# Performance work log

Measured on AMD Instinct MI355X. Metric: run time of the kernel, lower is better.

Reference implementation:

```python
import jax, jax.numpy as jnp
import numpy as np


def setup_inputs() -> dict:
    key = jax.random.key(0)
    k1, k2, k3 = jax.random.split(key, 3)
    N, F, C, E = 100000, 256, 64, 3200000
    x = jax.random.normal(k1, (N, F), dtype=jnp.float32)
    edge_index = jax.random.randint(k2, (2, E), 0, N, dtype=jnp.int64)
    W = jax.random.normal(k3, (F, C), dtype=jnp.float32) * (1.0 / np.sqrt(F))
    b = jnp.zeros((C,), dtype=jnp.float32)
    return {"x": x, "edge_index": edge_index, "W": W, "b": b}


def reference(x, edge_index, W, b):
    N = x.shape[0]
    # Linear transform first (GCNConv: x @ W)
    xw = x @ W  # [N, C]
    # gcn_norm: add self-loops with weight 1
    loops = jnp.arange(N, dtype=edge_index.dtype)
    src = jnp.concatenate([edge_index[0], loops])
    dst = jnp.concatenate([edge_index[1], loops])
    ones = jnp.ones(src.shape[0], dtype=xw.dtype)
    deg = jax.ops.segment_sum(ones, dst, num_segments=N)  # in-degree incl. self-loop
    deg_inv_sqrt = jnp.where(deg > 0, jax.lax.rsqrt(deg), 0.0)
    norm = deg_inv_sqrt[src] * deg_inv_sqrt[dst]  # [E+N]
    # Message: norm * x_j, then MEAN aggregation over destinations (aggr='mean')
    msg = xw[src] * norm[:, None]  # [E+N, C]
    agg = jax.ops.segment_sum(msg, dst, num_segments=N)  # [N, C]
    cnt = jnp.maximum(deg, 1.0)  # number of incoming messages per node
    out = agg / cnt[:, None] + b
    return jax.nn.log_softmax(out, axis=1)
```

## Files before the change

### kernel.cpp

```cpp
#include <hip/hip_runtime.h>


#define C_DIM 64
#define F_DIM 256
#define TILE 128
#define BIN_PT 16
#define BIN_TILE_E 4096
#define SORT_CAP 6144

#if __has_builtin(__builtin_amdgcn_cvt_pk_f32_fp8) && __has_builtin(__builtin_amdgcn_cvt_pk_fp8_f32)
#define USE_FP8 1
#endif

typedef __attribute__((ext_vector_type(8))) short bf16x8;
typedef __attribute__((ext_vector_type(2))) short bf16x2;
typedef __attribute__((ext_vector_type(4))) float f32x4;
typedef __attribute__((ext_vector_type(2))) float f32x2;

static __device__ __forceinline__ unsigned short f2bf(float f) {
    unsigned int u = __float_as_uint(f);
    unsigned int r = (u + 0x7FFFu + ((u >> 16) & 1u)) >> 16;
    return (unsigned short)r;
}
static __device__ __forceinline__ float u2lo(unsigned int u) {
    return __uint_as_float(u << 16);
}
static __device__ __forceinline__ float u2hi(unsigned int u) {
    return __uint_as_float(u & 0xFFFF0000u);
}

#if !defined(USE_FP8)
#if __has_builtin(__builtin_amdgcn_fdot2_f32_bf16)
static __device__ __forceinline__ void acc_pair(unsigned int u, float& lo, float& hi) {
    union { unsigned int ui; bf16x2 v; } p;
    p.ui = u;
    const bf16x2 SEL_LO = { (short)0x3F80, (short)0 };
    const bf16x2 SEL_HI = { (short)0, (short)0x3F80 };
    lo = __builtin_amdgcn_fdot2_f32_bf16(p.v, SEL_LO, lo, false);
    hi = __builtin_amdgcn_fdot2_f32_bf16(p.v, SEL_HI, hi, false);
}
#else
static __device__ __forceinline__ void acc_pair(unsigned int u, float& lo, float& hi) {
    lo += u2lo(u);
    hi += u2hi(u);
}
#endif
#endif


__global__ void k_zero1(int* __restrict__ a, int N) {
    int i = blockIdx.x * blockDim.x + threadIdx.x;
    if (i < N) a[i] = 0;
}

__global__ void k_zero2(int* __restrict__ a, int* __restrict__ b, int N) {
    int i = blockIdx.x * blockDim.x + threadIdx.x;
    if (i < N) { a[i] = 0; b[i] = 0; }
}

__global__ void k_count(const int* __restrict__ ei, int* __restrict__ degE, int E) {
    int stride = gridDim.x * blockDim.x;
    for (int e = blockIdx.x * blockDim.x + threadIdx.x; e < E; e += stride)
        atomicAdd(&degE[ei[E + e]], 1);
}

__global__ void k_dis2(const int* __restrict__ degE, float* __restrict__ dis, int N) {
    int i = blockIdx.x * blockDim.x + threadIdx.x;
    if (i < N) dis[i] = rsqrtf((float)(degE[i] + 1));
}


__global__ void k_prep(const float* __restrict__ W, unsigned short* __restrict__ Wt,
                       int* __restrict__ gcur, int K) {
    int i = blockIdx.x * blockDim.x + threadIdx.x;
    int c = i & 63, k = i >> 6;
    Wt[(size_t)c * F_DIM + k] = f2bf(W[(size_t)k * C_DIM + c]);
    if (i < K) gcur[i] = i * SORT_CAP;
}


__launch_bounds__(256)
__global__ void k_bin(const int* __restrict__ ei, int* __restrict__ gcur,
                      unsigned int* __restrict__ colb, int E, int K, int nTiles) {
    __shared__ int hcnt[1024];
    __shared__ int hoff[1024];
    __shared__ int gbase[1024];
    __shared__ int wps[4];
    __shared__ unsigned int stage[BIN_TILE_E];
    __shared__ unsigned short stage_bk[BIN_TILE_E];
    const int t = threadIdx.x;
    const int wv = t >> 6;
    const int ln = t & 63;

    for (int tile = blockIdx.x; tile < nTiles; tile += gridDim.x) {
        const int e0 = tile * BIN_TILE_E;
        const int nE = min(BIN_TILE_E, E - e0);
        hcnt[t] = 0; hcnt[t + 256] = 0; hcnt[t + 512] = 0; hcnt[t + 768] = 0;
        __syncthreads();

        unsigned int pk[BIN_PT];
        int bk[BIN_PT];
        int off[BIN_PT];
        #pragma unroll
        for (int j = 0; j < BIN_PT; ++j) {
            int e = e0 + j * 256 + t;
            if (e < E) {
                int s = ei[e];
                int d = ei[E + e];
                int k = d >> 7;
                bk[j]  = k;
                pk[j]  = ((unsigned)(d & 127) << 25) | (unsigned)s;
                off[j] = atomicAdd(&hcnt[k], 1);
            } else bk[j] = -1;
        }
        __syncthreads();

        int a0 = hcnt[t*4], a1 = hcnt[t*4+1], a2 = hcnt[t*4+2], a3 = hcnt[t*4+3];
        int s4 = a0 + a1 + a2 + a3;
        int incl = s4;
        #pragma unroll
        for (int o = 1; o < 64; o <<= 1) {
            int u = __shfl_up(incl, o, 64);
            if (ln >= o) incl += u;
        }
        if (ln == 63) wps[wv] = incl;
        __syncthreads();
        int wpre = 0;
        #pragma unroll
        for (int w = 0; w < 4; ++w)
            if (w < wv) wpre += wps[w];
        int eb = wpre + incl - s4;
        hoff[t*4+0] = eb;
        hoff[t*4+1] = eb + a0;
        hoff[t*4+2] = eb + a0 + a1;
        hoff[t*4+3] = eb + a0 + a1 + a2;
        __syncthreads();

        #pragma unroll
        for (int j = 0; j < BIN_PT; ++j)
            if (bk[j] >= 0) {
                int p = hoff[bk[j]] + off[j];
                stage[p] = pk[j];
                stage_bk[p] = (unsigned short)bk[j];
            }

        for (int kq = t; kq < K; kq += 256) {
            int c = hcnt[kq];
            gbase[kq] = (c > 0) ? atomicAdd(&gcur[kq], c) : 0;
        }
        __syncthreads();

        for (int i = t; i < nE; i += 256) {
            int bb = stage_bk[i];
            int idx = gbase[bb] + (i - hoff[bb]);
            if (idx < (bb + 1) * SORT_CAP)
                colb[idx] = stage[i];
        }
        __syncthreads();
    }
}


__launch_bounds__(256)
__global__ void k_sort(unsigned int* __restrict__ colb,
                       const int* __restrict__ gcur,
                       int* __restrict__ rowptr, int* __restrict__ rowcnt,
                       float* __restrict__ dis, int N, int K) {
    __shared__ unsigned int scache[SORT_CAP];
    __shared__ int ncnt[TILE];
    __shared__ int nscan[TILE];
    __shared__ int ncur[TILE];
    const int t = threadIdx.x;
    const int k = blockIdx.x;
    const int base = k * SORT_CAP;
    const int cnt  = min(gcur[k] - base, SORT_CAP);
    const int node0 = k << 7;

    if (t < TILE) ncnt[t] = 0;
    __syncthreads();
    for (int i = t; i < cnt; i += 256) {
        unsigned int pk = colb[base + i];
        scache[i] = pk;
        atomicAdd(&ncnt[pk >> 25], 1);
    }
    __syncthreads();

    if (t < TILE) nscan[t] = ncnt[t];
    __syncthreads();
    for (int o = 1; o < TILE; o <<= 1) {
        int v = 0;
        if (t < TILE && t >= o) v = nscan[t - o];
        __syncthreads();
        if (t < TILE) nscan[t] += v;
        __syncthreads();
    }
    if (t < TILE) {
        int ex = nscan[t] - ncnt[t];
        ncur[t] = ex;
        int node = node0 + t;
        if (node < N) {
            rowptr[node] = base + ex;
            rowcnt[node] = ncnt[t];
            dis[node] = rsqrtf((float)(ncnt[t] + 1));
        }
    }
    __syncthreads();

    for (int i = t; i < cnt; i += 256) {
        unsigned int pk = scache[i];
        int dl  = (int)(pk >> 25);
        int pos = atomicAdd(&ncur[dl], 1);
        colb[base + pos] = pk & 0x1FFFFFFu;
    }
}


__launch_bounds__(256)
__global__ void k_gemm_mfma(const float* __restrict__ x,
                            const unsigned short* __restrict__ Wt,
                            const float* __restrict__ dis,
                            void* __restrict__ yout, int N) {
    __shared__ float4 xs2[2][1024];
    const int t    = threadIdx.x;
    const int wv   = t >> 6;
    const int lane = t & 63;
    const int lr   = lane & 15;
    const int lq   = lane >> 4;
    const int row0 = blockIdx.x * 64;

    auto stagefn = [&](int buf, int kk) {
        #pragma unroll
        for (int j = 0; j < 4; ++j) {
            int base_idx = j * 256 + wv * 64;
            int idx = base_idx + lane;
            int r   = idx >> 4;
            int c4  = idx & 15;
            int sc4 = c4 ^ (r & 15);
            int gr  = row0 + r;
            if (gr >= N) gr = N - 1;
            const float* g = x + (size_t)gr * F_DIM + kk * 64 + sc4 * 4;
            float4* lbase = &xs2[buf][base_idx];
            __builtin_amdgcn_global_load_lds(
                (const __attribute__((address_space(1))) unsigned int*)g,
                (__attribute__((address_space(3))) unsigned int*)lbase,
                16, 0, 0);
        }
    };

    f32x4 acc[4] = {};

    stagefn(0, 0);
    __syncthreads();

    for (int kk = 0; kk < 4; ++kk) {
        if (kk < 3) stagefn((kk + 1) & 1, kk + 1);

        const float4* rowp = &xs2[kk & 1][(wv * 16 + lr) * 16];
        #pragma unroll
        for (int kc2 = 0; kc2 < 2; ++kc2) {
            int c4 = kc2 * 8 + lq * 2;
            float4 f0 = rowp[c4 ^ lr];
            float4 f1 = rowp[(c4 + 1) ^ lr];
            union { bf16x8 v; unsigned int u[4]; } a;
            a.u[0] = (unsigned)f2bf(f0.x) | ((unsigned)f2bf(f0.y) << 16);
            a.u[1] = (unsigned)f2bf(f0.z) | ((unsigned)f2bf(f0.w) << 16);
            a.u[2] = (unsigned)f2bf(f1.x) | ((unsigned)f2bf(f1.y) << 16);
            a.u[3] = (unsigned)f2bf(f1.z) | ((unsigned)f2bf(f1.w) << 16);
            const int kglob = kk * 64 + kc2 * 32 + lq * 8;
            #pragma unroll
            for (int cb = 0; cb < 4; ++cb) {
                bf16x8 bfr = *(const bf16x8*)(Wt + (size_t)(cb * 16 + lr) * F_DIM + kglob);
                acc[cb] = __builtin_amdgcn_mfma_f32_16x16x32_bf16(a.v, bfr, acc[cb], 0, 0, 0);
            }
        }
        __syncthreads();
    }

    const int rbase = row0 + wv * 16 + lq * 4;
    #pragma unroll
    for (int j = 0; j < 4; ++j) {
        int r = rbase + j;
        if (r < N) {
            float dd = dis[r];
#ifdef USE_FP8
            unsigned char* yf = (unsigned char*)yout;
            #pragma unroll
            for (int cb = 0; cb < 4; ++cb) {
                float v = acc[cb][j] * dd;
                int p = __builtin_amdgcn_cvt_pk_fp8_f32(v, v, 0, false);
                yf[(size_t)r * C_DIM + cb * 16 + lr] = (unsigned char)(p & 0xFF);
            }
#else
            unsigned short* ybp = (unsigned short*)yout;
            #pragma unroll
            for (int cb = 0; cb < 4; ++cb)
                ybp[(size_t)r * C_DIM + cb * 16 + lr] = f2bf(acc[cb][j] * dd);
#endif
        }
    }
}


__launch_bounds__(256)
__global__ void k_agg(const int* __restrict__ rowptr, const int* __restrict__ rowcnt,
                      const int* __restrict__ col,
                      const void* __restrict__ yin, const float* __restrict__ dis,
                      const float* __restrict__ b, float* __restrict__ out, int N) {
    const int lane = threadIdx.x & 63;
    const int g    = lane >> 3;
    const int cl   = lane & 7;
    int row = blockIdx.x * 4 + (threadIdx.x >> 6);
    if (row >= N) return;
    const int start = rowptr[row];
    const int cntE  = rowcnt[row];
    const int end   = start + cntE;

    float a0, a1, a2, a3, a4, a5, a6, a7;

#ifdef USE_FP8
    const uint2* yv = (const uint2*)yin;
    f32x2 p01 = {0.f, 0.f}, p23 = {0.f, 0.f}, p45 = {0.f, 0.f}, p67 = {0.f, 0.f};
    if (g == 0) {
        uint2 u = yv[(size_t)row * 8 + cl];
        p01 = __builtin_amdgcn_cvt_pk_f32_fp8((int)u.x, false);
        p23 = __builtin_amdgcn_cvt_pk_f32_fp8((int)u.x, true);
        p45 = __builtin_amdgcn_cvt_pk_f32_fp8((int)u.y, false);
        p67 = __builtin_amdgcn_cvt_pk_f32_fp8((int)u.y, true);
    }
    int i = start + g;
    for (; i + 24 < end; i += 32) {
        int s[4];
        #pragma unroll
        for (int j = 0; j < 4; ++j) s[j] = col[i + 8 * j];
        uint2 v[4];
        #pragma unroll
        for (int j = 0; j < 4; ++j) v[j] = yv[(size_t)s[j] * 8 + cl];
        #pragma unroll
        for (int j = 0; j < 4; ++j) {
            p01 += __builtin_amdgcn_cvt_pk_f32_fp8((int)v[j].x, false);
            p23 += __builtin_amdgcn_cvt_pk_f32_fp8((int)v[j].x, true);
            p45 += __builtin_amdgcn_cvt_pk_f32_fp8((int)v[j].y, false);
            p67 += __builtin_amdgcn_cvt_pk_f32_fp8((int)v[j].y, true);
        }
    }
    for (; i < end; i += 8) {
        uint2 u = yv[(size_t)col[i] * 8 + cl];
        p01 += __builtin_amdgcn_cvt_pk_f32_fp8((int)u.x, false);
        p23 += __builtin_amdgcn_cvt_pk_f32_fp8((int)u.x, true);
        p45 += __builtin_amdgcn_cvt_pk_f32_fp8((int)u.y, false);
        p67 += __builtin_amdgcn_cvt_pk_f32_fp8((int)u.y, true);
    }
    a0 = p01.x; a1 = p01.y; a2 = p23.x; a3 = p23.y;
    a4 = p45.x; a5 = p45.y; a6 = p67.x; a7 = p67.y;
#else
    const uint4* yv = (const uint4*)yin;
    a0 = a1 = a2 = a3 = a4 = a5 = a6 = a7 = 0.f;
    if (g == 0) {
        uint4 u = yv[(size_t)row * 8 + cl];
        a0 = u2lo(u.x); a1 = u2hi(u.x); a2 = u2lo(u.y); a3 = u2hi(u.y);
        a4 = u2lo(u.z); a5 = u2hi(u.z); a6 = u2lo(u.w); a7 = u2hi(u.w);
    }
    int i = start + g;
    for (; i + 24 < end; i += 32) {
        int s[4];
        #pragma unroll
        for (int j = 0; j < 4; ++j) s[j] = col[i + 8 * j];
        uint4 v[4];
        #pragma unroll
        for (int j = 0; j < 4; ++j) v[j] = yv[(size_t)s[j] * 8 + cl];
        #pragma unroll
        for (int j = 0; j < 4; ++j) {
            acc_pair(v[j].x, a0, a1);
            acc_pair(v[j].y, a2, a3);
            acc_pair(v[j].z, a4, a5);
            acc_pair(v[j].w, a6, a7);
        }
    }
    for (; i < end; i += 8) {
        uint4 u = yv[(size_t)col[i] * 8 + cl];
        acc_pair(u.x, a0, a1);
        acc_pair(u.y, a2, a3);
        acc_pair(u.z, a4, a5);
        acc_pair(u.w, a6, a7);
    }
#endif

    #pragma unroll
    for (int o = 8; o <= 32; o <<= 1) {
        a0 += __shfl_xor(a0, o, 64); a1 += __shfl_xor(a1, o, 64);
        a2 += __shfl_xor(a2, o, 64); a3 += __shfl_xor(a3, o, 64);
        a4 += __shfl_xor(a4, o, 64); a5 += __shfl_xor(a5, o, 64);
        a6 += __shfl_xor(a6, o, 64); a7 += __shfl_xor(a7, o, 64);
    }

    const float scale = dis[row] / (float)(cntE + 1);
    const float4 b0 = *(const float4*)&b[8 * cl];
    const float4 b1 = *(const float4*)&b[8 * cl + 4];
    float v0 = a0 * scale + b0.x;
    float v1 = a1 * scale + b0.y;
    float v2 = a2 * scale + b0.z;
    float v3 = a3 * scale + b0.w;
    float v4 = a4 * scale + b1.x;
    float v5 = a5 * scale + b1.y;
    float v6 = a6 * scale + b1.z;
    float v7 = a7 * scale + b1.w;

    float m = fmaxf(fmaxf(fmaxf(v0, v1), fmaxf(v2, v3)),
                    fmaxf(fmaxf(v4, v5), fmaxf(v6, v7)));
    #pragma unroll
    for (int o = 4; o >= 1; o >>= 1) m = fmaxf(m, __shfl_xor(m, o, 64));
    float ss = __expf(v0 - m) + __expf(v1 - m) + __expf(v2 - m) + __expf(v3 - m)
             + __expf(v4 - m) + __expf(v5 - m) + __expf(v6 - m) + __expf(v7 - m);
    #pragma unroll
    for (int o = 4; o >= 1; o >>= 1) ss += __shfl_xor(ss, o, 64);
    float lg = logf(ss);

    if (g == 0) {
        float* orow = out + (size_t)row * C_DIM + 8 * cl;
        *(float4*)(orow + 0) = make_float4(v0 - m - lg, v1 - m - lg, v2 - m - lg, v3 - m - lg);
        *(float4*)(orow + 4) = make_float4(v4 - m - lg, v5 - m - lg, v6 - m - lg, v7 - m - lg);
    }
}


__launch_bounds__(256, 4)
__global__ void k_gemmF(const float* __restrict__ x, const float* __restrict__ W,
                        const float* __restrict__ dis, float* __restrict__ y, int N) {
    __shared__ float xs[64 * 68];
    __shared__ float ws[64 * 64];
    const int t   = threadIdx.x;
    const int c16 = t & 15;
    const int rg  = t >> 4;
    const int row0 = blockIdx.x * 64;

    float acc[4][4] = {};

    for (int kk = 0; kk < F_DIM / 64; ++kk) {
        {
            int r  = t >> 2;
            int fq = (t & 3) * 16;
            int grow = row0 + r;
            float4 v0, v1, v2, v3;
            if (grow < N) {
                const float* src = x + (long long)grow * F_DIM + kk * 64 + fq;
                v0 = *(const float4*)(src + 0);
                v1 = *(const float4*)(src + 4);
                v2 = *(const float4*)(src + 8);
                v3 = *(const float4*)(src + 12);
            } else {
                v0 = v1 = v2 = v3 = make_float4(0.f, 0.f, 0.f, 0.f);
            }
            float4* dstp = (float4*)&xs[r * 68 + fq];
            dstp[0] = v0; dstp[1] = v1; dstp[2] = v2; dstp[3] = v3;
        }
        {
            int f  = t >> 2;
            int cq = (t & 3) * 16;
            const float* src = W + (long long)(kk * 64 + f) * C_DIM + cq;
            float4* dstp = (float4*)&ws[f * 64 + cq];
            dstp[0] = *(const float4*)(src + 0);
            dstp[1] = *(const float4*)(src + 4);
            dstp[2] = *(const float4*)(src + 8);
            dstp[3] = *(const float4*)(src + 12);
        }
        __syncthreads();

        const float4* xs4 = (const float4*)xs;
        const float4* ws4 = (const float4*)ws;
        #pragma unroll
        for (int f4 = 0; f4 < 16; ++f4) {
            float xr[4][4];
            #pragma unroll
            for (int k = 0; k < 4; ++k) {
                float4 v = xs4[(rg * 4 + k) * 17 + f4];
                xr[k][0] = v.x; xr[k][1] = v.y; xr[k][2] = v.z; xr[k][3] = v.w;
            }
            #pragma unroll
            for (int j = 0; j < 4; ++j) {
                float4 wv = ws4[(f4 * 4 + j) * 16 + c16];
                #pragma unroll
                for (int k = 0; k < 4; ++k) {
                    acc[k][0] += xr[k][j] * wv.x;
                    acc[k][1] += xr[k][j] * wv.y;
                    acc[k][2] += xr[k][j] * wv.z;
                    acc[k][3] += xr[k][j] * wv.w;
                }
            }
        }
        __syncthreads();
    }

    const int c = c16 * 4;
    #pragma unroll
    for (int k = 0; k < 4; ++k) {
        int row = row0 + rg * 4 + k;
        if (row < N) {
            float dd = dis[row];
            float4 v = make_float4(acc[k][0]*dd, acc[k][1]*dd, acc[k][2]*dd, acc[k][3]*dd);
            *(float4*)&y[(size_t)row * C_DIM + c] = v;
        }
    }
}

__global__ void k_scan_blk(const int* __restrict__ degE, int* __restrict__ excl,
                           int* __restrict__ bsum, int N) {
    __shared__ int sm[1024];
    const int tid = threadIdx.x;
    int i = blockIdx.x * 1024 + tid;
    int v = (i < N) ? degE[i] : 0;
    sm[tid] = v;
    __syncthreads();
    for (int off = 1; off < 1024; off <<= 1) {
        int t = (tid >= off) ? sm[tid - off] : 0;
        __syncthreads();
        sm[tid] += t;
        __syncthreads();
    }
    int incl = sm[tid];
    if (i < N) excl[i] = incl - v;
    if (tid == 1023) bsum[blockIdx.x] = incl;
}

__global__ void k_scan_top(int* __restrict__ bs, int nblk) {
    __shared__ int sm[128];
    const int tid = threadIdx.x;
    int v = (tid < nblk) ? bs[tid] : 0;
    sm[tid] = v;
    __syncthreads();
    for (int off = 1; off < 128; off <<= 1) {
        int t = (tid >= off) ? sm[tid - off] : 0;
        __syncthreads();
        sm[tid] += t;
        __syncthreads();
    }
    if (tid < nblk) bs[tid] = sm[tid] - v;
}

__global__ void k_scan_add(const int* __restrict__ excl, const int* __restrict__ bs,
                           int* __restrict__ rowptr, int N, int E) {
    int i = blockIdx.x * blockDim.x + threadIdx.x;
    if (i < N) rowptr[i] = excl[i] + bs[i >> 10];
    if (i == 0) rowptr[N] = E;
}

__global__ void k_scatter(const int* __restrict__ ei, const int* __restrict__ rowptr,
                          int* __restrict__ cnt, int* __restrict__ col, int E) {
    int stride = gridDim.x * blockDim.x;
    for (int e = blockIdx.x * blockDim.x + threadIdx.x; e < E; e += stride) {
        int s = ei[e];
        int d = ei[E + e];
        int p = atomicAdd(&cnt[d], 1);
        col[rowptr[d] + p] = s;
    }
}

__global__ void k_aggB(const int* __restrict__ rowptr, const int* __restrict__ col,
                       const float* __restrict__ y, const float* __restrict__ dis,
                       const float* __restrict__ b, float* __restrict__ out, int N) {
    const int lane = threadIdx.x & 63;
    int row = blockIdx.x * 4 + (threadIdx.x >> 6);
    if (row >= N) return;
    const int start = rowptr[row], end = rowptr[row + 1];
    float acc = y[(size_t)row * C_DIM + lane];
    for (int i = start; i < end; ++i) acc += y[(size_t)col[i] * C_DIM + lane];
    float val = acc * dis[row] / (float)(end - start + 1) + b[lane];
    float m = val;
    #pragma unroll
    for (int o = 32; o >= 1; o >>= 1) m = fmaxf(m, __shfl_xor(m, o, 64));
    float ex = expf(val - m);
    float ss = ex;
    #pragma unroll
    for (int o = 32; o >= 1; o >>= 1) ss += __shfl_xor(ss, o, 64);
    out[(size_t)row * C_DIM + lane] = val - m - logf(ss);
}

__global__ void k_selfloop2(const float* __restrict__ y, const float* __restrict__ dis,
                            float* __restrict__ agg, int NC) {
    int i = blockIdx.x * blockDim.x + threadIdx.x;
    if (i < NC) agg[i] = dis[i >> 6] * y[i];
}

__launch_bounds__(256)
__global__ void k_edge2(const int* __restrict__ ei, const float* __restrict__ y,
                        const float* __restrict__ dis, float* __restrict__ agg, int E) {
    const int lane = threadIdx.x & 63;
    int wid = (blockIdx.x * blockDim.x + threadIdx.x) >> 6;
    int nw  = (gridDim.x * blockDim.x) >> 6;
    for (int e = wid; e < E; e += nw) {
        int s = ei[e];
        int d = ei[E + e];
        atomicAdd(&agg[(size_t)d * C_DIM + lane], y[(size_t)s * C_DIM + lane] * dis[d]);
    }
}

__launch_bounds__(256)
__global__ void k_final2(float* __restrict__ agg, const int* __restrict__ degE,
                         const float* __restrict__ b, int N) {
    const int lane = threadIdx.x & 63;
    int row = blockIdx.x * 4 + (threadIdx.x >> 6);
    if (row >= N) return;
    float v = agg[(size_t)row * C_DIM + lane] / (float)(degE[row] + 1) + b[lane];
    float m = v;
    #pragma unroll
    for (int o = 32; o >= 1; o >>= 1) m = fmaxf(m, __shfl_xor(m, o, 64));
    float ex = expf(v - m);
    float ss = ex;
    #pragma unroll
    for (int o = 32; o >= 1; o >>= 1) ss += __shfl_xor(ss, o, 64);
    agg[(size_t)row * C_DIM + lane] = v - m - logf(ss);
}


extern "C" void kernel_launch(void* const* d_in, const int* in_sizes, int n_in,
                              void* d_out, int out_size, void* d_ws, size_t ws_size,
                              hipStream_t stream) {
    const float* x  = (const float*)d_in[0];
    const int*   ei = (const int*)d_in[1];
    const float* W  = (const float*)d_in[2];
    const float* b  = (const float*)d_in[3];

    const int C = in_sizes[3];
    const int F = in_sizes[2] / C;
    const int N = in_sizes[0] / F;
    const int E = in_sizes[1] / 2;

    float* out = (float*)d_out;
    char*  wsb = (char*)d_ws;

    const int K    = (N + TILE - 1) / TILE;
    const int nblk = (N + 1023) / 1024;

    size_t offA = 0;
    void*  yv   = (void*)(wsb + offA);    offA += ((size_t)N * C * 2 + 15) & ~15ull;
    unsigned short* Wt = (unsigned short*)(wsb + offA); offA += ((size_t)F * C * 2 + 15) & ~15ull;
    float* disA   = (float*)(wsb + offA); offA += (size_t)N * 4;
    int*   rowptrA= (int*)(wsb + offA);   offA += (size_t)N * 4;
    int*   rowcntA= (int*)(wsb + offA);   offA += (size_t)N * 4;
    int*   gcur   = (int*)(wsb + offA);   offA += (size_t)K * 4;
    unsigned int* colb = (unsigned int*)(wsb + offA); offA += (size_t)K * SORT_CAP * 4;

    size_t offB = 0;
    float* yB     = (float*)(wsb + offB); offB += (size_t)N * C * 4;
    float* disB   = (float*)(wsb + offB); offB += (size_t)N * 4;
    int*   rowptrB= (int*)(wsb + offB);   offB += ((size_t)N + 1) * 4;
    int*   degE   = (int*)(wsb + offB);   offB += (size_t)N * 4;
    int*   cntB   = (int*)(wsb + offB);   offB += (size_t)N * 4;
    int*   excl   = (int*)(wsb + offB);   offB += (size_t)nblk * 1024 * 4;
    int*   bsum   = (int*)(wsb + offB);   offB += 128 * 4;
    int*   colB   = (int*)(wsb + offB);   offB += (size_t)E * 4;

    const bool okA = (offA <= ws_size) && (K <= 1024) && (N < (1 << 25)) &&
                     (C == 64) && (F == 256) &&
                     ((long long)E < (long long)K * SORT_CAP);
    const bool okB = (offB <= ws_size) && (nblk <= 128);

    const dim3 B256(256);
    const dim3 gN((N + 255) / 256);
    const int nTiles = (E + BIN_TILE_E - 1) / BIN_TILE_E;
    const int gemmBlocks = (N + 63) / 64;

    if (okA) {
        hipLaunchKernelGGL(k_prep,      dim3((F * C + 255) / 256), B256, 0, stream,
                           W, Wt, gcur, K);
        hipLaunchKernelGGL(k_bin,       dim3(nTiles), B256, 0, stream, ei, gcur, colb,
                           E, K, nTiles);
        hipLaunchKernelGGL(k_sort,      dim3(K), B256, 0, stream, colb, gcur,
                           rowptrA, rowcntA, disA, N, K);
        hipLaunchKernelGGL(k_gemm_mfma, dim3(gemmBlocks), B256, 0, stream,
                           x, Wt, disA, yv, N);
        hipLaunchKernelGGL(k_agg,       dim3((N + 3) / 4), B256, 0, stream,
                           rowptrA, rowcntA, (const int*)colb,
                           (const void*)yv, disA, b, out, N);
    } else if (okB) {
        hipLaunchKernelGGL(k_zero2,    gN, B256, 0, stream, degE, cntB, N);
        hipLaunchKernelGGL(k_count,    dim3(2048), B256, 0, stream, ei, degE, E);
        hipLaunchKernelGGL(k_dis2,     gN, B256, 0, stream, degE, disB, N);
        hipLaunchKernelGGL(k_scan_blk, dim3(nblk), dim3(1024), 0, stream, degE, excl, bsum, N);
        hipLaunchKernelGGL(k_scan_top, dim3(1), dim3(128), 0, stream, bsum, nblk);
        hipLaunchKernelGGL(k_scan_add, gN, B256, 0, stream, excl, bsum, rowptrB, N, E);
        hipLaunchKernelGGL(k_gemmF,    dim3(gemmBlocks), B256, 0, stream, x, W, disB, yB, N);
        hipLaunchKernelGGL(k_scatter,  dim3(2048), B256, 0, stream, ei, rowptrB, cntB, colB, E);
        hipLaunchKernelGGL(k_aggB,     dim3((N + 3) / 4), B256, 0, stream,
                           rowptrB, colB, yB, disB, b, out, N);
    } else {
        hipLaunchKernelGGL(k_zero1,     gN, B256, 0, stream, degE, N);
        hipLaunchKernelGGL(k_count,     dim3(2048), B256, 0, stream, ei, degE, E);
        hipLaunchKernelGGL(k_dis2,      gN, B256, 0, stream, degE, disB, N);
        hipLaunchKernelGGL(k_gemmF,     dim3(gemmBlocks), B256, 0, stream, x, W, disB, yB, N);
        hipLaunchKernelGGL(k_selfloop2, dim3(((size_t)N * C + 255) / 256), B256, 0, stream,
                           yB, disB, out, N * C);
        hipLaunchKernelGGL(k_edge2,     dim3(4096), B256, 0, stream, ei, yB, disB, out, E);
        hipLaunchKernelGGL(k_final2,    dim3((N + 3) / 4), B256, 0, stream, out, degE, b, N);
    }
}
```

Before: 161.4 us.

## Run GEMM before binning and apply degree scaling to projected rows inside sort

The MFMA GEMM no longer depends on the degree normalisation, so it now runs right after weight prep and before edge binning and sorting. The per-row deg^-1/2 scaling of the projected features moves into the sort kernel, which rescales its tile's 128 rows in place after computing degrees. This removes the GEMM's dependency on the sort output and may leave the freshly rescaled rows warm in cache for aggregation. The cost is an extra read-modify-write pass over the projected features. In the FP8 path it also adds a second quantisation round, which increases rounding error.

```diff
diff --git a/kernel.cpp b/kernel.cpp
--- a/kernel.cpp
+++ b/kernel.cpp
@@ -80,145 +80,8 @@
 
 
 __launch_bounds__(256)
-__global__ void k_bin(const int* __restrict__ ei, int* __restrict__ gcur,
-                      unsigned int* __restrict__ colb, int E, int K, int nTiles) {
-    __shared__ int hcnt[1024];
-    __shared__ int hoff[1024];
-    __shared__ int gbase[1024];
-    __shared__ int wps[4];
-    __shared__ unsigned int stage[BIN_TILE_E];
-    __shared__ unsigned short stage_bk[BIN_TILE_E];
-    const int t = threadIdx.x;
-    const int wv = t >> 6;
-    const int ln = t & 63;
-
-    for (int tile = blockIdx.x; tile < nTiles; tile += gridDim.x) {
-        const int e0 = tile * BIN_TILE_E;
-        const int nE = min(BIN_TILE_E, E - e0);
-        hcnt[t] = 0; hcnt[t + 256] = 0; hcnt[t + 512] = 0; hcnt[t + 768] = 0;
-        __syncthreads();
-
-        unsigned int pk[BIN_PT];
-        int bk[BIN_PT];
-        int off[BIN_PT];
-        #pragma unroll
-        for (int j = 0; j < BIN_PT; ++j) {
-            int e = e0 + j * 256 + t;
-            if (e < E) {
-                int s = ei[e];
-                int d = ei[E + e];
-                int k = d >> 7;
-                bk[j]  = k;
-                pk[j]  = ((unsigned)(d & 127) << 25) | (unsigned)s;
-                off[j] = atomicAdd(&hcnt[k], 1);
-            } else bk[j] = -1;
-        }
-        __syncthreads();
-
-        int a0 = hcnt[t*4], a1 = hcnt[t*4+1], a2 = hcnt[t*4+2], a3 = hcnt[t*4+3];
-        int s4 = a0 + a1 + a2 + a3;
-        int incl = s4;
-        #pragma unroll
-        for (int o = 1; o < 64; o <<= 1) {
-            int u = __shfl_up(incl, o, 64);
-            if (ln >= o) incl += u;
-        }
-        if (ln == 63) wps[wv] = incl;
-        __syncthreads();
-        int wpre = 0;
-        #pragma unroll
-        for (int w = 0; w < 4; ++w)
-            if (w < wv) wpre += wps[w];
-        int eb = wpre + incl - s4;
-        hoff[t*4+0] = eb;
-        hoff[t*4+1] = eb + a0;
-        hoff[t*4+2] = eb + a0 + a1;
-        hoff[t*4+3] = eb + a0 + a1 + a2;
-        __syncthreads();
-
-        #pragma unroll
-        for (int j = 0; j < BIN_PT; ++j)
-            if (bk[j] >= 0) {
-                int p = hoff[bk[j]] + off[j];
-                stage[p] = pk[j];
-                stage_bk[p] = (unsigned short)bk[j];
-            }
-
-        for (int kq = t; kq < K; kq += 256) {
-            int c = hcnt[kq];
-            gbase[kq] = (c > 0) ? atomicAdd(&gcur[kq], c) : 0;
-        }
-        __syncthreads();
-
-        for (int i = t; i < nE; i += 256) {
-            int bb = stage_bk[i];
-            int idx = gbase[bb] + (i - hoff[bb]);
-            if (idx < (bb + 1) * SORT_CAP)
-                colb[idx] = stage[i];
-        }
-        __syncthreads();
-    }
-}
-
-
-__launch_bounds__(256)
-__global__ void k_sort(unsigned int* __restrict__ colb,
-                       const int* __restrict__ gcur,
-                       int* __restrict__ rowptr, int* __restrict__ rowcnt,
-                       float* __restrict__ dis, int N, int K) {
-    __shared__ unsigned int scache[SORT_CAP];
-    __shared__ int ncnt[TILE];
-    __shared__ int nscan[TILE];
-    __shared__ int ncur[TILE];
-    const int t = threadIdx.x;
-    const int k = blockIdx.x;
-    const int base = k * SORT_CAP;
-    const int cnt  = min(gcur[k] - base, SORT_CAP);
-    const int node0 = k << 7;
-
-    if (t < TILE) ncnt[t] = 0;
-    __syncthreads();
-    for (int i = t; i < cnt; i += 256) {
-        unsigned int pk = colb[base + i];
-        scache[i] = pk;
-        atomicAdd(&ncnt[pk >> 25], 1);
-    }
-    __syncthreads();
-
-    if (t < TILE) nscan[t] = ncnt[t];
-    __syncthreads();
-    for (int o = 1; o < TILE; o <<= 1) {
-        int v = 0;
-        if (t < TILE && t >= o) v = nscan[t - o];
-        __syncthreads();
-        if (t < TILE) nscan[t] += v;
-        __syncthreads();
-    }
-    if (t < TILE) {
-        int ex = nscan[t] - ncnt[t];
-        ncur[t] = ex;
-        int node = node0 + t;
-        if (node < N) {
-            rowptr[node] = base + ex;
-            rowcnt[node] = ncnt[t];
-            dis[node] = rsqrtf((float)(ncnt[t] + 1));
-        }
-    }
-    __syncthreads();
-
-    for (int i = t; i < cnt; i += 256) {
-        unsigned int pk = scache[i];
-        int dl  = (int)(pk >> 25);
-        int pos = atomicAdd(&ncur[dl], 1);
-        colb[base + pos] = pk & 0x1FFFFFFu;
-    }
-}
-
-
-__launch_bounds__(256)
 __global__ void k_gemm_mfma(const float* __restrict__ x,
                             const unsigned short* __restrict__ Wt,
-                            const float* __restrict__ dis,
                             void* __restrict__ yout, int N) {
     __shared__ float4 xs2[2][1024];
     const int t    = threadIdx.x;
@@ -281,12 +144,11 @@
     for (int j = 0; j < 4; ++j) {
         int r = rbase + j;
         if (r < N) {
-            float dd = dis[r];
 #ifdef USE_FP8
             unsigned char* yf = (unsigned char*)yout;
             #pragma unroll
             for (int cb = 0; cb < 4; ++cb) {
-                float v = acc[cb][j] * dd;
+                float v = acc[cb][j];
                 int p = __builtin_amdgcn_cvt_pk_fp8_f32(v, v, 0, false);
                 yf[(size_t)r * C_DIM + cb * 16 + lr] = (unsigned char)(p & 0xFF);
             }
@@ -294,10 +156,176 @@
             unsigned short* ybp = (unsigned short*)yout;
             #pragma unroll
             for (int cb = 0; cb < 4; ++cb)
-                ybp[(size_t)r * C_DIM + cb * 16 + lr] = f2bf(acc[cb][j] * dd);
+                ybp[(size_t)r * C_DIM + cb * 16 + lr] = f2bf(acc[cb][j]);
 #endif
         }
     }
+}
+
+
+__launch_bounds__(256)
+__global__ void k_bin(const int* __restrict__ ei, int* __restrict__ gcur,
+                      unsigned int* __restrict__ colb, int E, int K, int nTiles) {
+    __shared__ int hcnt[1024];
+    __shared__ int hoff[1024];
+    __shared__ int gbase[1024];
+    __shared__ int wps[4];
+    __shared__ unsigned int stage[BIN_TILE_E];
+    __shared__ unsigned short stage_bk[BIN_TILE_E];
+    const int t = threadIdx.x;
+    const int wv = t >> 6;
+    const int ln = t & 63;
+
+    for (int tile = blockIdx.x; tile < nTiles; tile += gridDim.x) {
+        const int e0 = tile * BIN_TILE_E;
+        const int nE = min(BIN_TILE_E, E - e0);
+        hcnt[t] = 0; hcnt[t + 256] = 0; hcnt[t + 512] = 0; hcnt[t + 768] = 0;
+        __syncthreads();
+
+        unsigned int pk[BIN_PT];
+        int bk[BIN_PT];
+        int off[BIN_PT];
+        #pragma unroll
+        for (int j = 0; j < BIN_PT; ++j) {
+            int e = e0 + j * 256 + t;
+            if (e < E) {
+                int s = ei[e];
+                int d = ei[E + e];
+                int k = d >> 7;
+                bk[j]  = k;
+                pk[j]  = ((unsigned)(d & 127) << 25) | (unsigned)s;
+                off[j] = atomicAdd(&hcnt[k], 1);
+            } else bk[j] = -1;
+        }
+        __syncthreads();
+
+        int a0 = hcnt[t*4], a1 = hcnt[t*4+1], a2 = hcnt[t*4+2], a3 = hcnt[t*4+3];
+        int s4 = a0 + a1 + a2 + a3;
+        int incl = s4;
+        #pragma unroll
+        for (int o = 1; o < 64; o <<= 1) {
+            int u = __shfl_up(incl, o, 64);
+            if (ln >= o) incl += u;
+        }
+        if (ln == 63) wps[wv] = incl;
+        __syncthreads();
+        int wpre = 0;
+        #pragma unroll
+        for (int w = 0; w < 4; ++w)
+            if (w < wv) wpre += wps[w];
+        int eb = wpre + incl - s4;
+        hoff[t*4+0] = eb;
+        hoff[t*4+1] = eb + a0;
+        hoff[t*4+2] = eb + a0 + a1;
+        hoff[t*4+3] = eb + a0 + a1 + a2;
+        __syncthreads();
+
+        #pragma unroll
+        for (int j = 0; j < BIN_PT; ++j)
+            if (bk[j] >= 0) {
+                int p = hoff[bk[j]] + off[j];
+                stage[p] = pk[j];
+                stage_bk[p] = (unsigned short)bk[j];
+            }
+
+        for (int kq = t; kq < K; kq += 256) {
+            int c = hcnt[kq];
+            gbase[kq] = (c > 0) ? atomicAdd(&gcur[kq], c) : 0;
+        }
+        __syncthreads();
+
+        for (int i = t; i < nE; i += 256) {
+            int bb = stage_bk[i];
+            int idx = gbase[bb] + (i - hoff[bb]);
+            if (idx < (bb + 1) * SORT_CAP)
+                colb[idx] = stage[i];
+        }
+        __syncthreads();
+    }
+}
+
+
+__launch_bounds__(256)
+__global__ void k_sort(unsigned int* __restrict__ colb,
+                       const int* __restrict__ gcur,
+                       int* __restrict__ rowptr, int* __restrict__ rowcnt,
+                       float* __restrict__ dis,
+                       unsigned int* __restrict__ yw,
+                       int N, int K) {
+    __shared__ unsigned int scache[SORT_CAP];
+    __shared__ int ncnt[TILE];
+    __shared__ int nscan[TILE];
+    __shared__ int ncur[TILE];
+    __shared__ float sdis[TILE];
+    const int t = threadIdx.x;
+    const int k = blockIdx.x;
+    const int base = k * SORT_CAP;
+    const int cnt  = min(gcur[k] - base, SORT_CAP);
+    const int node0 = k << 7;
+
+    if (t < TILE) ncnt[t] = 0;
+    __syncthreads();
+    for (int i = t; i < cnt; i += 256) {
+        unsigned int pk = colb[base + i];
+        scache[i] = pk;
+        atomicAdd(&ncnt[pk >> 25], 1);
+    }
+    __syncthreads();
+
+    if (t < TILE) nscan[t] = ncnt[t];
+    __syncthreads();
+    for (int o = 1; o < TILE; o <<= 1) {
+        int v = 0;
+        if (t < TILE && t >= o) v = nscan[t - o];
+        __syncthreads();
+        if (t < TILE) nscan[t] += v;
+        __syncthreads();
+    }
+    if (t < TILE) {
+        int ex = nscan[t] - ncnt[t];
+        ncur[t] = ex;
+        int node = node0 + t;
+        if (node < N) {
+            rowptr[node] = base + ex;
+            rowcnt[node] = ncnt[t];
+            float d = rsqrtf((float)(ncnt[t] + 1));
+            dis[node] = d;
+            sdis[t] = d;
+        }
+    }
+    __syncthreads();
+
+    for (int i = t; i < cnt; i += 256) {
+        unsigned int pk = scache[i];
+        int dl  = (int)(pk >> 25);
+        int pos = atomicAdd(&ncur[dl], 1);
+        colb[base + pos] = pk & 0x1FFFFFFu;
+    }
+
+    const int nrows = min(TILE, N - node0);
+#ifdef USE_FP8
+    unsigned int* yrow = yw + (size_t)node0 * 16;
+    for (int u = t; u < nrows * 16; u += 256) {
+        int r = u >> 4;
+        float d = sdis[r];
+        unsigned int v = yrow[u];
+        f32x2 lo = __builtin_amdgcn_cvt_pk_f32_fp8((int)v, false);
+        f32x2 hi = __builtin_amdgcn_cvt_pk_f32_fp8((int)v, true);
+        int p = __builtin_amdgcn_cvt_pk_fp8_f32(lo.x * d, lo.y * d, 0, false);
+        p = __builtin_amdgcn_cvt_pk_fp8_f32(hi.x * d, hi.y * d, p, true);
+        yrow[u] = (unsigned int)p;
+    }
+#else
+    unsigned int* yrow = yw + (size_t)node0 * 32;
+    for (int u = t; u < nrows * 32; u += 256) {
+        int r = u >> 5;
+        unsigned int v = yrow[u];
+        float d = sdis[r];
+        unsigned short lo = f2bf(u2lo(v) * d);
+        unsigned short hi = f2bf(u2hi(v) * d);
+        yrow[u] = ((unsigned int)hi << 16) | lo;
+    }
+#endif
 }
 
 
@@ -662,12 +690,12 @@
     if (okA) {
         hipLaunchKernelGGL(k_prep,      dim3((F * C + 255) / 256), B256, 0, stream,
                            W, Wt, gcur, K);
+        hipLaunchKernelGGL(k_gemm_mfma, dim3(gemmBlocks), B256, 0, stream,
+                           x, Wt, yv, N);
         hipLaunchKernelGGL(k_bin,       dim3(nTiles), B256, 0, stream, ei, gcur, colb,
                            E, K, nTiles);
         hipLaunchKernelGGL(k_sort,      dim3(K), B256, 0, stream, colb, gcur,
-                           rowptrA, rowcntA, disA, N, K);
-        hipLaunchKernelGGL(k_gemm_mfma, dim3(gemmBlocks), B256, 0, stream,
-                           x, Wt, disA, yv, N);
+                           rowptrA, rowcntA, disA, (unsigned int*)yv, N, K);
         hipLaunchKernelGGL(k_agg,       dim3((N + 3) / 4), B256, 0, stream,
                            rowptrA, rowcntA, (const int*)colb,
                            (const void*)yv, disA, b, out, N);
```

After: 163.3 us. No clear change (+1.2%).
